# Kernel optimization log

Measured on AMD Instinct MI355X. Metric: run time of the kernel, lower is better.

## Reference

```python
import jax, jax.numpy as jnp
import numpy as np

NEG_SLOPE = 0.2  # PyG GATConv default negative_slope


def _gat_layer(x, src, dst, W, a_src, a_dst, b, num_nodes):
    # x: [N, Fin] -> h: [N, Fout]
    h = x @ W
    # per-node attention logits (heads=1)
    alpha_s = h @ a_src  # [N]
    alpha_d = h @ a_dst  # [N]
    # edge scores e_ij = LeakyReLU(a_src . h_j + a_dst . h_i), j=src, i=dst
    e = alpha_s[src] + alpha_d[dst]
    e = jnp.where(e >= 0, e, NEG_SLOPE * e)
    # segment softmax over edges sharing the same destination node
    e_max = jax.ops.segment_max(e, dst, num_segments=num_nodes)  # [N]
    w = jnp.exp(e - e_max[dst])  # [E]
    denom = jax.ops.segment_sum(w, dst, num_segments=num_nodes)  # [N]
    alpha = w / denom[dst]  # [E]
    # weighted scatter-sum of source messages into destinations
    out = jax.ops.segment_sum(h[src] * alpha[:, None], dst, num_segments=num_nodes)
    return out + b


def _add_self_loops(edge_index, num_nodes):
    loops = jnp.arange(num_nodes, dtype=edge_index.dtype)
    src = jnp.concatenate([edge_index[0], loops])
    dst = jnp.concatenate([edge_index[1], loops])
    return src, dst


def setup_inputs() -> dict:
    key = jax.random.key(0)
    ks = jax.random.split(key, 8)
    N, E, F_in, F_hid, F_out = 50000, 800000, 128, 128, 64
    inp = {
        "node_features": jax.random.normal(ks[0], (N, F_in), dtype=jnp.float32),
        "edge_index": jax.random.randint(ks[1], (2, E), 0, N, dtype=jnp.int32),
        "W1": jax.random.normal(ks[2], (F_in, F_hid), dtype=jnp.float32) / np.sqrt(F_in),
        "a_src1": jax.random.normal(ks[3], (F_hid,), dtype=jnp.float32) / np.sqrt(F_hid),
        "a_dst1": jax.random.normal(ks[4], (F_hid,), dtype=jnp.float32) / np.sqrt(F_hid),
        "b1": jnp.zeros((F_hid,), dtype=jnp.float32),
        "W2": jax.random.normal(ks[5], (F_hid, F_out), dtype=jnp.float32) / np.sqrt(F_hid),
        "a_src2": jax.random.normal(ks[6], (F_out,), dtype=jnp.float32) / np.sqrt(F_out),
        "a_dst2": jax.random.normal(ks[7], (F_out,), dtype=jnp.float32) / np.sqrt(F_out),
        "b2": jnp.zeros((F_out,), dtype=jnp.float32),
    }
    return inp


def reference(node_features, edge_index, W1, a_src1, a_dst1, b1, W2, a_src2, a_dst2, b2):
    num_nodes = node_features.shape[0]
    src, dst = _add_self_loops(edge_index, num_nodes)
    x = _gat_layer(node_features, src, dst, W1, a_src1, a_dst1, b1, num_nodes)
    x = jax.nn.relu(x)
    x = _gat_layer(x, src, dst, W2, a_src2, a_dst2, b2, num_nodes)
    return x
```

## Files before the change

kernel.cpp:

```cpp
#include <hip/hip_runtime.h>
#include <hip/hip_fp16.h>
#include <cstddef>

#define NEG_SLOPE 0.2f
#define TILE 4096
#define CSR_CAP 6144

__device__ __forceinline__ float leaky(float x) { return x >= 0.f ? x : NEG_SLOPE * x; }

__device__ __forceinline__ int wave_iscan(int v, int lane) {
#pragma unroll
    for (int off = 1; off < 64; off <<= 1) {
        int t = __shfl_up(v, off);
        if (lane >= off) v += t;
    }
    return v;
}

template <int F, typename IT>
__global__ __launch_bounds__(16 * (F / 8)) void gemm_alpha(
    const IT* __restrict__ x, const float* __restrict__ W,
    const float* __restrict__ a_s, const float* __restrict__ a_d,
    __half* __restrict__ hh, float* __restrict__ alphaS, float* __restrict__ alphaD,
    int N)
{
    constexpr int K = 128;
    constexpr int BK = 32;
    constexpr int BM = 64;
    constexpr int TM = 4;
    constexpr int TN = 8;
    constexpr int TC = F / TN;
    constexpr int THREADS = 16 * TC;

    __shared__ float As[BK][BM + 4];
    __shared__ float Bs[BK][F + 4];

    const int tid = threadIdx.x;
    const int tr = tid / TC;
    const int tc = tid % TC;
    const int rowb = blockIdx.x * BM;
    const int c0 = tc * 4;
    const int c1 = tc * 4 + F / 2;

    float acc[TM][TN];
#pragma unroll
    for (int m = 0; m < TM; m++)
#pragma unroll
        for (int n = 0; n < TN; n++) acc[m][n] = 0.f;

    for (int kt = 0; kt < K / BK; kt++) {
        for (int i = tid; i < BM * (BK / 4); i += THREADS) {
            int c4 = i & 7, r = i >> 3;
            int gr = rowb + r;
            float4 v = make_float4(0.f, 0.f, 0.f, 0.f);
            if (gr < N) {
                if constexpr (sizeof(IT) == 4) {
                    v = *(const float4*)((const float*)x + (size_t)gr * K + kt * BK + c4 * 4);
                } else {
                    const __half2* xp = (const __half2*)((const __half*)x + (size_t)gr * K + kt * BK + c4 * 4);
                    float2 f0 = __half22float2(xp[0]);
                    float2 f1 = __half22float2(xp[1]);
                    v = make_float4(f0.x, f0.y, f1.x, f1.y);
                }
            }
            As[c4 * 4 + 0][r] = v.x;
            As[c4 * 4 + 1][r] = v.y;
            As[c4 * 4 + 2][r] = v.z;
            As[c4 * 4 + 3][r] = v.w;
        }
        for (int i = tid; i < BK * (F / 4); i += THREADS) {
            int r = i / (F / 4), c4 = i % (F / 4);
            *(float4*)&Bs[r][c4 * 4] = *(const float4*)(W + (size_t)(kt * BK + r) * F + c4 * 4);
        }
        __syncthreads();

#pragma unroll 8
        for (int k = 0; k < BK; k++) {
            float a[TM], b[TN];
            *(float4*)&a[0] = *(float4*)&As[k][tr * 4];
            *(float4*)&b[0] = *(float4*)&Bs[k][c0];
            *(float4*)&b[4] = *(float4*)&Bs[k][c1];
#pragma unroll
            for (int m = 0; m < TM; m++)
#pragma unroll
                for (int n = 0; n < TN; n++)
                    acc[m][n] += a[m] * b[n];
        }
        __syncthreads();
    }

    float asv[TN], adv[TN];
    *(float4*)&asv[0] = *(const float4*)(a_s + c0);
    *(float4*)&asv[4] = *(const float4*)(a_s + c1);
    *(float4*)&adv[0] = *(const float4*)(a_d + c0);
    *(float4*)&adv[4] = *(const float4*)(a_d + c1);

#pragma unroll
    for (int m = 0; m < TM; m++) {
        int row = rowb + tr * 4 + m;
        bool ok = (row < N);
        if (ok) {
            __half2 h0 = __floats2half2_rn(acc[m][0], acc[m][1]);
            __half2 h1 = __floats2half2_rn(acc[m][2], acc[m][3]);
            __half2 h2 = __floats2half2_rn(acc[m][4], acc[m][5]);
            __half2 h3 = __floats2half2_rn(acc[m][6], acc[m][7]);
            __half2* hp0 = (__half2*)(hh + (size_t)row * F + c0);
            __half2* hp1 = (__half2*)(hh + (size_t)row * F + c1);
            hp0[0] = h0; hp0[1] = h1;
            hp1[0] = h2; hp1[1] = h3;
        }
        float ps = 0.f, pd = 0.f;
#pragma unroll
        for (int n = 0; n < TN; n++) {
            ps += acc[m][n] * asv[n];
            pd += acc[m][n] * adv[n];
        }
#pragma unroll
        for (int off = TC / 2; off >= 1; off >>= 1) {
            ps += __shfl_down(ps, off, TC);
            pd += __shfl_down(pd, off, TC);
        }
        if (ok && tc == 0) { alphaS[row] = ps; alphaD[row] = pd; }
    }
}

__global__ __launch_bounds__(256) void bucket_count(
    const int* __restrict__ dst, int* __restrict__ gcnt, int E)
{
    __shared__ int lcnt[256];
    const int tid = threadIdx.x;
    const int base = blockIdx.x * TILE;
    lcnt[tid] = 0;
    __syncthreads();
#pragma unroll
    for (int j = 0; j < TILE / 256; j++) {
        int idx = base + j * 256 + tid;
        if (idx < E) atomicAdd(&lcnt[dst[idx] >> 8], 1);
    }
    __syncthreads();
    int c = lcnt[tid];
    if (c > 0) atomicAdd(&gcnt[tid], c);
}

__global__ __launch_bounds__(256) void bucket_scan(
    const int* __restrict__ gcnt, int* __restrict__ gstart,
    int* __restrict__ gfill, int NB, int* __restrict__ rowptrN, int E)
{
    __shared__ int ws[4];
    int tid = threadIdx.x, lane = tid & 63, wid = tid >> 6;
    int v = (tid < NB) ? gcnt[tid] : 0;
    int incl = wave_iscan(v, lane);
    if (lane == 63) ws[wid] = incl;
    __syncthreads();
    int woff = 0;
    for (int w = 0; w < wid; w++) woff += ws[w];
    int excl = woff + incl - v;
    if (tid <= NB) gstart[tid] = excl;
    if (tid < NB) gfill[tid] = excl;
    if (tid == 255) gstart[256] = excl + v;
    if (tid == 0) *rowptrN = E;
}

__global__ __launch_bounds__(256) void bucket_scatter(
    const int* __restrict__ src, const int* __restrict__ dst,
    int* __restrict__ gfill, unsigned* __restrict__ staging, int E)
{
    __shared__ int lcnt[256];
    __shared__ int loff[256];
    __shared__ int gbase[256];
    __shared__ int ws[4];
    __shared__ unsigned pairs[TILE];
    __shared__ unsigned char bkt[TILE];

    const int tid = threadIdx.x;
    const int base = blockIdx.x * TILE;
    const int vt = min(TILE, E - base);

    lcnt[tid] = 0;
    __syncthreads();

    int d[TILE / 256], s[TILE / 256], r[TILE / 256];
#pragma unroll
    for (int j = 0; j < TILE / 256; j++) {
        int idx = base + j * 256 + tid;
        if (idx < E) {
            d[j] = dst[idx]; s[j] = src[idx];
            r[j] = atomicAdd(&lcnt[d[j] >> 8], 1);
        } else d[j] = -1;
    }
    __syncthreads();
    {
        int lane = tid & 63, wid = tid >> 6;
        int v = lcnt[tid];
        int incl = wave_iscan(v, lane);
        if (lane == 63) ws[wid] = incl;
        __syncthreads();
        int woff = 0;
        for (int w = 0; w < wid; w++) woff += ws[w];
        loff[tid] = woff + incl - v;
    }
    __syncthreads();
    {
        int c = lcnt[tid];
        if (c > 0) gbase[tid] = atomicAdd(&gfill[tid], c);
    }
    __syncthreads();
#pragma unroll
    for (int j = 0; j < TILE / 256; j++) {
        if (d[j] >= 0) {
            int b = d[j] >> 8;
            int slot = loff[b] + r[j];
            pairs[slot] = ((unsigned)d[j] << 16) | (unsigned)s[j];
            bkt[slot] = (unsigned char)b;
        }
    }
    __syncthreads();
    for (int slot = tid; slot < vt; slot += 256) {
        int b = bkt[slot];
        staging[gbase[b] + (slot - loff[b])] = pairs[slot];
    }
}

__global__ __launch_bounds__(256) void bucket_to_csr(
    const unsigned* __restrict__ staging, const int* __restrict__ gstart,
    int* __restrict__ rowptr, int* __restrict__ src_sorted, int N)
{
    __shared__ unsigned lp[CSR_CAP];
    __shared__ int lcnt[256], loff[256], lfill[256];
    __shared__ int ws[4];
    const int tid = threadIdx.x;
    const int b = blockIdx.x;
    const int beg = gstart[b], end = gstart[b + 1];
    const int len = end - beg;

    lcnt[tid] = 0;
    __syncthreads();
    for (int p = tid; p < len; p += 256) {
        unsigned u = staging[beg + p];
        if (p < CSR_CAP) lp[p] = u;
        atomicAdd(&lcnt[(u >> 16) & 255], 1);
    }
    __syncthreads();
    {
        int lane = tid & 63, wid = tid >> 6;
        int v = lcnt[tid];
        int incl = wave_iscan(v, lane);
        if (lane == 63) ws[wid] = incl;
        __syncthreads();
        int woff = 0;
        for (int w = 0; w < wid; w++) woff += ws[w];
        int excl = woff + incl - v;
        loff[tid] = excl;
        lfill[tid] = excl;
        int node = (b << 8) + tid;
        if (node < N) rowptr[node] = beg + excl;
    }
    __syncthreads();
    for (int p = tid; p < len; p += 256) {
        unsigned u = (p < CSR_CAP) ? lp[p] : staging[beg + p];
        int pos = atomicAdd(&lfill[(u >> 16) & 255], 1);
        src_sorted[beg + pos] = (int)(u & 0xFFFFu);
    }
}

template <int F, bool RELU, typename OT>
__global__ __launch_bounds__(256) void gat_aggregate(
    const int* __restrict__ rowptr, const int* __restrict__ src_sorted,
    const __half* __restrict__ hh, const float* __restrict__ aS,
    const float* __restrict__ aD, const float* __restrict__ bias,
    OT* __restrict__ out, int N)
{
    constexpr int LPE = F / 8;
    constexpr int EPW = 64 / LPE;

    const int i = blockIdx.x * 4 + (threadIdx.x >> 6);
    if (i >= N) return;
    const int lane = threadIdx.x & 63;
    const int sub = lane / LPE;
    const int l = lane % LPE;

    const float adi = aD[i];
    const int start = rowptr[i];
    const int end = rowptr[i + 1];

    float acc0[8], acc1[8];
#pragma unroll
    for (int q = 0; q < 8; q++) { acc0[q] = 0.f; acc1[q] = 0.f; }
    float den0 = 0.f, den1 = 0.f;

    int e0 = start + sub;
    int e1 = e0 + EPW;
    int s0 = (e0 < end) ? src_sorted[e0] : -1;
    int s1 = (e1 < end) ? src_sorted[e1] : -1;

    while (s0 >= 0) {
        int n0 = (e0 + 2 * EPW < end) ? src_sorted[e0 + 2 * EPW] : -1;
        int n1 = (e1 + 2 * EPW < end) ? src_sorted[e1 + 2 * EPW] : -1;
        {
            float w = __expf(leaky(aS[s0] + adi));
            uint4 u = *(const uint4*)(hh + (size_t)s0 * F + l * 8);
            const __half2* hp = (const __half2*)&u;
#pragma unroll
            for (int q = 0; q < 4; q++) {
                float2 f = __half22float2(hp[q]);
                acc0[q * 2]     += w * f.x;
                acc0[q * 2 + 1] += w * f.y;
            }
            den0 += w;
        }
        if (s1 >= 0) {
            float w = __expf(leaky(aS[s1] + adi));
            uint4 u = *(const uint4*)(hh + (size_t)s1 * F + l * 8);
            const __half2* hp = (const __half2*)&u;
#pragma unroll
            for (int q = 0; q < 4; q++) {
                float2 f = __half22float2(hp[q]);
                acc1[q * 2]     += w * f.x;
                acc1[q * 2 + 1] += w * f.y;
            }
            den1 += w;
        }
        e0 += 2 * EPW; e1 += 2 * EPW;
        s0 = n0; s1 = n1;
    }

    float acc[8];
#pragma unroll
    for (int q = 0; q < 8; q++) acc[q] = acc0[q] + acc1[q];
    float denom = den0 + den1;

#pragma unroll
    for (int off = 32; off >= LPE; off >>= 1) {
#pragma unroll
        for (int q = 0; q < 8; q++) acc[q] += __shfl_down(acc[q], off);
        denom += __shfl_down(denom, off);
    }

    if (sub == 0) {
        float wsf = __expf(leaky(aS[i] + adi));
        uint4 u = *(const uint4*)(hh + (size_t)i * F + l * 8);
        const __half2* hp = (const __half2*)&u;
        float inv = 1.f / (denom + wsf);
        float4 b0 = *(const float4*)(bias + l * 8);
        float4 b1 = *(const float4*)(bias + l * 8 + 4);
        float o[8];
#pragma unroll
        for (int q = 0; q < 4; q++) {
            float2 f = __half22float2(hp[q]);
            o[q * 2]     = (acc[q * 2]     + wsf * f.x) * inv;
            o[q * 2 + 1] = (acc[q * 2 + 1] + wsf * f.y) * inv;
        }
        o[0] += b0.x; o[1] += b0.y; o[2] += b0.z; o[3] += b0.w;
        o[4] += b1.x; o[5] += b1.y; o[6] += b1.z; o[7] += b1.w;
        if (RELU) {
#pragma unroll
            for (int q = 0; q < 8; q++) o[q] = fmaxf(o[q], 0.f);
        }
        if constexpr (sizeof(OT) == 2) {
            __half2 qh[4];
            qh[0] = __floats2half2_rn(o[0], o[1]);
            qh[1] = __floats2half2_rn(o[2], o[3]);
            qh[2] = __floats2half2_rn(o[4], o[5]);
            qh[3] = __floats2half2_rn(o[6], o[7]);
            *(uint4*)((__half*)out + (size_t)i * F + l * 8) = *(uint4*)qh;
        } else {
            *(float4*)((float*)out + (size_t)i * F + l * 8)     = make_float4(o[0], o[1], o[2], o[3]);
            *(float4*)((float*)out + (size_t)i * F + l * 8 + 4) = make_float4(o[4], o[5], o[6], o[7]);
        }
    }
}

extern "C" void kernel_launch(void* const* d_in, const int* in_sizes, int n_in,
                              void* d_out, int out_size, void* d_ws, size_t ws_size,
                              hipStream_t stream)
{
    const float* x   = (const float*)d_in[0];
    const int*   ei  = (const int*)d_in[1];
    const float* W1  = (const float*)d_in[2];
    const float* aS1 = (const float*)d_in[3];
    const float* aD1 = (const float*)d_in[4];
    const float* b1  = (const float*)d_in[5];
    const float* W2  = (const float*)d_in[6];
    const float* aS2 = (const float*)d_in[7];
    const float* aD2 = (const float*)d_in[8];
    const float* b2  = (const float*)d_in[9];

    const int K = 128, F1 = 128, F2 = 64;
    const int N = in_sizes[0] / K;
    const int E = in_sizes[1] / 2;
    const int* src = ei;
    const int* dst = ei + E;

    const int Np = (N + 4) & ~3;
    const int NB = (N + 255) >> 8;
    const int nbt = (E + TILE - 1) / TILE;

    char* wsb = (char*)d_ws;
    int* gcnt         = (int*)wsb;      wsb += 256 * 4;
    int* gstart       = (int*)wsb;      wsb += 264 * 4;
    int* gfill        = (int*)wsb;      wsb += 256 * 4;
    int* rowptr       = (int*)wsb;      wsb += (size_t)(Np + 4) * 4;
    unsigned* staging = (unsigned*)wsb; wsb += (size_t)E * 4;
    int* src_sorted   = (int*)wsb;      wsb += (size_t)E * 4;
    __half* hh1       = (__half*)wsb;   wsb += (size_t)N * F1 * 2;
    __half* x2h       = (__half*)wsb;   wsb += (size_t)N * F1 * 2;
    __half* hh2       = (__half*)wsb;   wsb += (size_t)N * F2 * 2;
    float* as_        = (float*)wsb;    wsb += (size_t)Np * 4;
    float* ad_        = (float*)wsb;    wsb += (size_t)Np * 4;

    hipMemsetAsync(gcnt, 0, 256 * 4, stream);

    dim3 blk(256);

    gemm_alpha<F1, float><<<dim3((N + 63) / 64), dim3(256), 0, stream>>>(
        x, W1, aS1, aD1, hh1, as_, ad_, N);

    bucket_count<<<dim3(nbt), blk, 0, stream>>>(dst, gcnt, E);
    bucket_scan<<<dim3(1), blk, 0, stream>>>(gcnt, gstart, gfill, NB, rowptr + N, E);
    bucket_scatter<<<dim3(nbt), blk, 0, stream>>>(src, dst, gfill, staging, E);
    bucket_to_csr<<<dim3(NB), blk, 0, stream>>>(staging, gstart, rowptr, src_sorted, N);

    gat_aggregate<F1, true, __half><<<dim3((N + 3) / 4), blk, 0, stream>>>(
        rowptr, src_sorted, hh1, as_, ad_, b1, x2h, N);

    gemm_alpha<F2, __half><<<dim3((N + 63) / 64), dim3(128), 0, stream>>>(
        x2h, W2, aS2, aD2, hh2, as_, ad_, N);
    gat_aggregate<F2, false, float><<<dim3((N + 3) / 4), blk, 0, stream>>>(
        rowptr, src_sorted, hh2, as_, ad_, b2, (float*)d_out, N);
}
```

Baseline: 227.2 us.

## Replace FP32 SIMT GEMM with FP16 MFMA 16x16x32 matrix-core kernel

Measured after the change: 202.3 us. 11.0% less time.

```diff
diff --git a/kernel.cpp b/kernel.cpp
--- a/kernel.cpp
+++ b/kernel.cpp
@@ -6,6 +6,10 @@
 #define TILE 4096
 #define CSR_CAP 6144
 
+typedef _Float16 h8 __attribute__((ext_vector_type(8)));
+typedef _Float16 h4 __attribute__((ext_vector_type(4)));
+typedef float f4 __attribute__((ext_vector_type(4)));
+
 __device__ __forceinline__ float leaky(float x) { return x >= 0.f ? x : NEG_SLOPE * x; }
 
 __device__ __forceinline__ int wave_iscan(int v, int lane) {
@@ -18,109 +22,92 @@
 }
 
 template <int F, typename IT>
-__global__ __launch_bounds__(16 * (F / 8)) void gemm_alpha(
+__global__ __launch_bounds__(256) void gemm_mfma(
     const IT* __restrict__ x, const float* __restrict__ W,
     const float* __restrict__ a_s, const float* __restrict__ a_d,
-    __half* __restrict__ hh, float* __restrict__ alphaS, float* __restrict__ alphaD,
+    _Float16* __restrict__ hh, float* __restrict__ alphaS, float* __restrict__ alphaD,
     int N)
 {
     constexpr int K = 128;
-    constexpr int BK = 32;
-    constexpr int BM = 64;
-    constexpr int TM = 4;
-    constexpr int TN = 8;
-    constexpr int TC = F / TN;
-    constexpr int THREADS = 16 * TC;
-
-    __shared__ float As[BK][BM + 4];
-    __shared__ float Bs[BK][F + 4];
+    constexpr int LDK = K + 8;
+    constexpr int NT = F / 16;
+
+    __shared__ _Float16 As[64 * LDK];
+    __shared__ _Float16 Wt[F * LDK];
 
     const int tid = threadIdx.x;
-    const int tr = tid / TC;
-    const int tc = tid % TC;
-    const int rowb = blockIdx.x * BM;
-    const int c0 = tc * 4;
-    const int c1 = tc * 4 + F / 2;
-
-    float acc[TM][TN];
-#pragma unroll
-    for (int m = 0; m < TM; m++)
-#pragma unroll
-        for (int n = 0; n < TN; n++) acc[m][n] = 0.f;
-
-    for (int kt = 0; kt < K / BK; kt++) {
-        for (int i = tid; i < BM * (BK / 4); i += THREADS) {
-            int c4 = i & 7, r = i >> 3;
+    const int wave = tid >> 6;
+    const int lane = tid & 63;
+    const int q = lane >> 4;
+    const int c = lane & 15;
+    const int rowb = blockIdx.x * 64;
+
+    if constexpr (sizeof(IT) == 4) {
+        for (int i = tid; i < 64 * (K / 4); i += 256) {
+            int r = i >> 5, c4 = i & 31;
             int gr = rowb + r;
-            float4 v = make_float4(0.f, 0.f, 0.f, 0.f);
-            if (gr < N) {
-                if constexpr (sizeof(IT) == 4) {
-                    v = *(const float4*)((const float*)x + (size_t)gr * K + kt * BK + c4 * 4);
-                } else {
-                    const __half2* xp = (const __half2*)((const __half*)x + (size_t)gr * K + kt * BK + c4 * 4);
-                    float2 f0 = __half22float2(xp[0]);
-                    float2 f1 = __half22float2(xp[1]);
-                    v = make_float4(f0.x, f0.y, f1.x, f1.y);
-                }
+            float4 v = (gr < N) ? *(const float4*)((const float*)x + (size_t)gr * K + c4 * 4)
+                                : make_float4(0.f, 0.f, 0.f, 0.f);
+            h4 hv = { (_Float16)v.x, (_Float16)v.y, (_Float16)v.z, (_Float16)v.w };
+            *(h4*)(As + r * LDK + c4 * 4) = hv;
+        }
+    } else {
+        for (int i = tid; i < 64 * (K / 8); i += 256) {
+            int r = i >> 4, c8 = i & 15;
+            int gr = rowb + r;
+            h8 v;
+            if (gr < N) v = *(const h8*)((const _Float16*)x + (size_t)gr * K + c8 * 8);
+            else        v = (h8)(_Float16)0.f;
+            *(h8*)(As + r * LDK + c8 * 8) = v;
+        }
+    }
+    for (int i = tid; i < K * F; i += 256) {
+        int k = i / F, n = i % F;
+        Wt[n * LDK + k] = (_Float16)W[i];
+    }
+    __syncthreads();
+
+    f4 acc[NT];
+#pragma unroll
+    for (int nt = 0; nt < NT; nt++) acc[nt] = (f4)0.f;
+
+    const _Float16* aw = As + (wave * 16 + c) * LDK + q * 8;
+#pragma unroll
+    for (int kt = 0; kt < 4; kt++) {
+        h8 af = *(const h8*)(aw + kt * 32);
+#pragma unroll
+        for (int nt = 0; nt < NT; nt++) {
+            h8 bf = *(const h8*)(Wt + (nt * 16 + c) * LDK + kt * 32 + q * 8);
+            acc[nt] = __builtin_amdgcn_mfma_f32_16x16x32_f16(af, bf, acc[nt], 0, 0, 0);
+        }
+    }
+
+    float asl[NT], adl[NT];
+#pragma unroll
+    for (int nt = 0; nt < NT; nt++) {
+        asl[nt] = a_s[nt * 16 + c];
+        adl[nt] = a_d[nt * 16 + c];
+    }
+    const int row0 = rowb + wave * 16 + q * 4;
+#pragma unroll
+    for (int r = 0; r < 4; r++) {
+        int row = row0 + r;
+        if (row < N) {
+            float ps = 0.f, pd = 0.f;
+#pragma unroll
+            for (int nt = 0; nt < NT; nt++) {
+                float v = acc[nt][r];
+                hh[(size_t)row * F + nt * 16 + c] = (_Float16)v;
+                ps += v * asl[nt];
+                pd += v * adl[nt];
             }
-            As[c4 * 4 + 0][r] = v.x;
-            As[c4 * 4 + 1][r] = v.y;
-            As[c4 * 4 + 2][r] = v.z;
-            As[c4 * 4 + 3][r] = v.w;
-        }
-        for (int i = tid; i < BK * (F / 4); i += THREADS) {
-            int r = i / (F / 4), c4 = i % (F / 4);
-            *(float4*)&Bs[r][c4 * 4] = *(const float4*)(W + (size_t)(kt * BK + r) * F + c4 * 4);
-        }
-        __syncthreads();
-
-#pragma unroll 8
-        for (int k = 0; k < BK; k++) {
-            float a[TM], b[TN];
-            *(float4*)&a[0] = *(float4*)&As[k][tr * 4];
-            *(float4*)&b[0] = *(float4*)&Bs[k][c0];
-            *(float4*)&b[4] = *(float4*)&Bs[k][c1];
-#pragma unroll
-            for (int m = 0; m < TM; m++)
-#pragma unroll
-                for (int n = 0; n < TN; n++)
-                    acc[m][n] += a[m] * b[n];
-        }
-        __syncthreads();
-    }
-
-    float asv[TN], adv[TN];
-    *(float4*)&asv[0] = *(const float4*)(a_s + c0);
-    *(float4*)&asv[4] = *(const float4*)(a_s + c1);
-    *(float4*)&adv[0] = *(const float4*)(a_d + c0);
-    *(float4*)&adv[4] = *(const float4*)(a_d + c1);
-
-#pragma unroll
-    for (int m = 0; m < TM; m++) {
-        int row = rowb + tr * 4 + m;
-        bool ok = (row < N);
-        if (ok) {
-            __half2 h0 = __floats2half2_rn(acc[m][0], acc[m][1]);
-            __half2 h1 = __floats2half2_rn(acc[m][2], acc[m][3]);
-            __half2 h2 = __floats2half2_rn(acc[m][4], acc[m][5]);
-            __half2 h3 = __floats2half2_rn(acc[m][6], acc[m][7]);
-            __half2* hp0 = (__half2*)(hh + (size_t)row * F + c0);
-            __half2* hp1 = (__half2*)(hh + (size_t)row * F + c1);
-            hp0[0] = h0; hp0[1] = h1;
-            hp1[0] = h2; hp1[1] = h3;
-        }
-        float ps = 0.f, pd = 0.f;
-#pragma unroll
-        for (int n = 0; n < TN; n++) {
-            ps += acc[m][n] * asv[n];
-            pd += acc[m][n] * adv[n];
-        }
-#pragma unroll
-        for (int off = TC / 2; off >= 1; off >>= 1) {
-            ps += __shfl_down(ps, off, TC);
-            pd += __shfl_down(pd, off, TC);
-        }
-        if (ok && tc == 0) { alphaS[row] = ps; alphaD[row] = pd; }
+#pragma unroll
+            for (int off = 8; off >= 1; off >>= 1) {
+                ps += __shfl_down(ps, off, 16);
+                pd += __shfl_down(pd, off, 16);
+            }
+            if (c == 0) { alphaS[row] = ps; alphaD[row] = pd; }
+        }
     }
 }
 
@@ -157,7 +144,6 @@
     int excl = woff + incl - v;
     if (tid <= NB) gstart[tid] = excl;
     if (tid < NB) gfill[tid] = excl;
-    if (tid == 255) gstart[256] = excl + v;
     if (tid == 0) *rowptrN = E;
 }
 
@@ -402,9 +388,9 @@
     int* rowptr       = (int*)wsb;      wsb += (size_t)(Np + 4) * 4;
     unsigned* staging = (unsigned*)wsb; wsb += (size_t)E * 4;
     int* src_sorted   = (int*)wsb;      wsb += (size_t)E * 4;
-    __half* hh1       = (__half*)wsb;   wsb += (size_t)N * F1 * 2;
-    __half* x2h       = (__half*)wsb;   wsb += (size_t)N * F1 * 2;
-    __half* hh2       = (__half*)wsb;   wsb += (size_t)N * F2 * 2;
+    _Float16* hh1     = (_Float16*)wsb; wsb += (size_t)N * F1 * 2;
+    _Float16* x2h     = (_Float16*)wsb; wsb += (size_t)N * F1 * 2;
+    _Float16* hh2     = (_Float16*)wsb; wsb += (size_t)N * F2 * 2;
     float* as_        = (float*)wsb;    wsb += (size_t)Np * 4;
     float* ad_        = (float*)wsb;    wsb += (size_t)Np * 4;
 
@@ -412,7 +398,7 @@
 
     dim3 blk(256);
 
-    gemm_alpha<F1, float><<<dim3((N + 63) / 64), dim3(256), 0, stream>>>(
+    gemm_mfma<F1, float><<<dim3((N + 63) / 64), blk, 0, stream>>>(
         x, W1, aS1, aD1, hh1, as_, ad_, N);
 
     bucket_count<<<dim3(nbt), blk, 0, stream>>>(dst, gcnt, E);
@@ -421,10 +407,10 @@
     bucket_to_csr<<<dim3(NB), blk, 0, stream>>>(staging, gstart, rowptr, src_sorted, N);
 
     gat_aggregate<F1, true, __half><<<dim3((N + 3) / 4), blk, 0, stream>>>(
-        rowptr, src_sorted, hh1, as_, ad_, b1, x2h, N);
-
-    gemm_alpha<F2, __half><<<dim3((N + 63) / 64), dim3(128), 0, stream>>>(
+        rowptr, src_sorted, (const __half*)hh1, as_, ad_, b1, (__half*)x2h, N);
+
+    gemm_mfma<F2, _Float16><<<dim3((N + 63) / 64), blk, 0, stream>>>(
         x2h, W2, aS2, aD2, hh2, as_, ad_, N);
     gat_aggregate<F2, false, float><<<dim3((N + 3) / 4), blk, 0, stream>>>(
-        rowptr, src_sorted, hh2, as_, ad_, b2, (float*)d_out, N);
-}
+        rowptr, src_sorted, (const __half*)hh2, as_, ad_, b2, (float*)d_out, N);
+}
```
